# Performance work log

Measured on AMD Instinct MI355X. Metric: run time of the kernel, lower is better.

Reference implementation:

```python
import jax, jax.numpy as jnp
import numpy as np

N = 50000      # nodes
E = 800000     # edges (before self-loops)
F_IN = 128     # input node features
H = 4          # attention heads
C = 32         # hidden channels per head (concat width = H*C = 128)
CLS = 40       # num classes (layer 4, concat=False -> mean over heads)
NEG_SLOPE = 0.2


def setup_inputs() -> dict:
    key = jax.random.key(0)
    ks = jax.random.split(key, 16)
    w = lambda k, shape: (jax.random.normal(k, shape, jnp.float32) * 0.1)
    return {
        "x": jax.random.normal(ks[0], (N, F_IN), jnp.float32),
        "edge_index": jax.random.randint(ks[1], (2, E), 0, N),
        "W1": w(ks[2], (F_IN, H * C)), "att_src1": w(ks[3], (H, C)), "att_dst1": w(ks[4], (H, C)), "b1": jnp.zeros((H * C,), jnp.float32),
        "W2": w(ks[5], (H * C, H * C)), "att_src2": w(ks[6], (H, C)), "att_dst2": w(ks[7], (H, C)), "b2": jnp.zeros((H * C,), jnp.float32),
        "W3": w(ks[8], (H * C, H * C)), "att_src3": w(ks[9], (H, C)), "att_dst3": w(ks[10], (H, C)), "b3": jnp.zeros((H * C,), jnp.float32),
        "W4": w(ks[11], (H * C, H * CLS)), "att_src4": w(ks[12], (H, CLS)), "att_dst4": w(ks[13], (H, CLS)), "b4": jnp.zeros((CLS,), jnp.float32),
    }


def _gat(x, W, a_src, a_dst, b, src, dst, n, heads, ch, concat):
    # Linear transform, per-head view: [n, heads, ch]
    h = (x @ W).reshape(n, heads, ch)
    # per-node scalar attention terms [n, heads]
    es = (h * a_src).sum(-1)
    ed = (h * a_dst).sum(-1)
    # edge logits: alpha_j (source) + alpha_i (target), leaky relu (PyG GATConv)
    e = jax.nn.leaky_relu(es[src] + ed[dst], NEG_SLOPE)  # [Etot, heads]
    # segment softmax over incoming edges of each dst node (self-loops guarantee >=1 edge)
    m = jax.ops.segment_max(e, dst, num_segments=n)
    ealpha = jnp.exp(e - m[dst])
    denom = jax.ops.segment_sum(ealpha, dst, num_segments=n)
    alpha = ealpha / denom[dst]
    # weighted message aggregation (scatter-add)
    out = jax.ops.segment_sum(h[src] * alpha[:, :, None], dst, num_segments=n)
    out = out.reshape(n, heads * ch) if concat else out.mean(axis=1)
    return out + b


def reference(x, edge_index, W1, att_src1, att_dst1, b1, W2, att_src2, att_dst2, b2,
              W3, att_src3, att_dst3, b3, W4, att_src4, att_dst4, b4):
    n = x.shape[0]
    loop = jnp.arange(n)
    src = jnp.concatenate([edge_index[0], loop])  # add self-loops (PyG default)
    dst = jnp.concatenate([edge_index[1], loop])
    # dropout layers are identity in eval mode (training=False)
    h = _gat(x, W1, att_src1, att_dst1, b1, src, dst, n, H, C, True)
    h = jax.nn.relu(h)
    h = _gat(h, W2, att_src2, att_dst2, b2, src, dst, n, H, C, True)
    h = jax.nn.relu(h)
    h = _gat(h, W3, att_src3, att_dst3, b3, src, dst, n, H, C, True)
    h = jax.nn.relu(h)
    h = _gat(h, W4, att_src4, att_dst4, b4, src, dst, n, H, CLS, False)
    return h
```

## Files before the change

kernel.cpp:

```cpp
#include <hip/hip_runtime.h>
#include <math.h>

#define NN 50000
#define EE 800000
#define ET (EE + NN)
#define NCHK ((NN + 255) / 256)
#define NEG 0.2f

__device__ __forceinline__ float lrelu(float x) { return x > 0.f ? x : NEG * x; }

typedef __bf16 bf16x8 __attribute__((ext_vector_type(8)));
typedef float f32x4 __attribute__((ext_vector_type(4)));


__global__ __launch_bounds__(256) void k_init_cnt(int* cnt) {
    int i = blockIdx.x * 256 + threadIdx.x;
    if (i < NN) cnt[i] = 1;
}

__global__ __launch_bounds__(256) void k_hist(const int* __restrict__ eidx, int* __restrict__ cnt) {
    int i = blockIdx.x * 256 + threadIdx.x;
    if (i < EE) atomicAdd(&cnt[eidx[EE + i]], 1);
}

__global__ __launch_bounds__(256) void k_csum(const int* __restrict__ cnt, int* __restrict__ csums) {
    __shared__ int sh[256];
    int t = threadIdx.x, i = blockIdx.x * 256 + t;
    sh[t] = (i < NN) ? cnt[i] : 0;
    __syncthreads();
    for (int off = 128; off > 0; off >>= 1) {
        if (t < off) sh[t] += sh[t + off];
        __syncthreads();
    }
    if (t == 0) csums[blockIdx.x] = sh[0];
}

__global__ __launch_bounds__(256) void k_cscan(int* __restrict__ csums, int* __restrict__ rowptr) {
    __shared__ int sh[256];
    int t = threadIdx.x;
    sh[t] = (t < NCHK) ? csums[t] : 0;
    __syncthreads();
    for (int off = 1; off < 256; off <<= 1) {
        int x = (t >= off) ? sh[t - off] : 0;
        __syncthreads();
        sh[t] += x;
        __syncthreads();
    }
    int ex = (t == 0) ? 0 : sh[t - 1];
    if (t < NCHK) csums[t] = ex;
    if (t == 0) rowptr[NN] = ET;
}

__global__ __launch_bounds__(256) void k_chscan(const int* __restrict__ cnt, const int* __restrict__ csums,
                                                int* __restrict__ rowptr, int* __restrict__ cursor) {
    __shared__ int sh[256];
    int t = threadIdx.x, b = blockIdx.x, i = b * 256 + t;
    int v = (i < NN) ? cnt[i] : 0;
    sh[t] = v;
    __syncthreads();
    for (int off = 1; off < 256; off <<= 1) {
        int x = (t >= off) ? sh[t - off] : 0;
        __syncthreads();
        sh[t] += x;
        __syncthreads();
    }
    int ex = (t == 0 ? 0 : sh[t - 1]) + csums[b];
    if (i < NN) { rowptr[i] = ex; cursor[i] = ex; }
}

__global__ __launch_bounds__(256) void k_scatter(const int* __restrict__ eidx,
                                                 int* __restrict__ cursor, int* __restrict__ ssrc) {
    int i = blockIdx.x * 256 + threadIdx.x;
    if (i >= ET) return;
    int s, d;
    if (i < EE) { s = eidx[i]; d = eidx[EE + i]; } else { s = d = i - EE; }
    int pos = atomicAdd(&cursor[d], 1);
    ssrc[pos] = s;
}


template <int NOUT>
__global__ __launch_bounds__(256) void k_gemm_mfma(const float* __restrict__ X,
                                                   const float* __restrict__ Wm,
                                                   float* __restrict__ Y) {
    constexpr int NT = NOUT / 16;
    __shared__ __bf16 WH[4][NOUT][8];
    __shared__ __bf16 WL[4][NOUT][8];
    int tid = threadIdx.x;
    int w = tid >> 6, l = tid & 63;
    int rb = blockIdx.x * 64;
    int arow = rb + w * 16 + (l & 15);
    int rclamp = arow < NN ? arow : NN - 1;
    int kg = l >> 4;
    f32x4 acc[NT];
    #pragma unroll
    for (int t = 0; t < NT; ++t) acc[t] = (f32x4){0.f, 0.f, 0.f, 0.f};

    for (int kc = 0; kc < 128; kc += 32) {
        for (int idx = tid; idx < 32 * NOUT; idx += 256) {
            int kk = idx / NOUT;
            int c  = idx - kk * NOUT;
            float v = Wm[(size_t)(kc + kk) * NOUT + c];
            __bf16 hi = (__bf16)v;
            __bf16 lo = (__bf16)(v - (float)hi);
            WH[kk >> 3][c][kk & 7] = hi;
            WL[kk >> 3][c][kk & 7] = lo;
        }
        __syncthreads();

        float4 aA = *reinterpret_cast<const float4*>(&X[(size_t)rclamp * 128 + kc + kg * 8]);
        float4 aB = *reinterpret_cast<const float4*>(&X[(size_t)rclamp * 128 + kc + kg * 8 + 4]);
        float av[8] = {aA.x, aA.y, aA.z, aA.w, aB.x, aB.y, aB.z, aB.w};
        bf16x8 ahi, alo;
        #pragma unroll
        for (int j = 0; j < 8; ++j) {
            __bf16 h = (__bf16)av[j];
            ahi[j] = h;
            alo[j] = (__bf16)(av[j] - (float)h);
        }

        #pragma unroll
        for (int t = 0; t < NT; ++t) {
            bf16x8 bhi = *reinterpret_cast<const bf16x8*>(&WH[kg][t * 16 + (l & 15)][0]);
            bf16x8 blo = *reinterpret_cast<const bf16x8*>(&WL[kg][t * 16 + (l & 15)][0]);
            acc[t] = __builtin_amdgcn_mfma_f32_16x16x32_bf16(ahi, bhi, acc[t], 0, 0, 0);
            acc[t] = __builtin_amdgcn_mfma_f32_16x16x32_bf16(alo, bhi, acc[t], 0, 0, 0);
            acc[t] = __builtin_amdgcn_mfma_f32_16x16x32_bf16(ahi, blo, acc[t], 0, 0, 0);
        }
        __syncthreads();
    }

    #pragma unroll
    for (int t = 0; t < NT; ++t) {
        int cc = t * 16 + (l & 15);
        #pragma unroll
        for (int i = 0; i < 4; ++i) {
            int rr = rb + w * 16 + (l >> 4) * 4 + i;
            if (rr < NN) Y[(size_t)rr * NOUT + cc] = acc[t][i];
        }
    }
}


template <int CH>
__global__ __launch_bounds__(256) void k_attn_scal(const float* __restrict__ Hf,
                                                   const float* __restrict__ asrc,
                                                   const float* __restrict__ adst,
                                                   float* __restrict__ es, float* __restrict__ ed) {
    int i = blockIdx.x * 256 + threadIdx.x;
    if (i >= NN * 4) return;
    int h = i & 3, n = i >> 2;
    const float4* row = reinterpret_cast<const float4*>(Hf + (size_t)n * (4 * CH) + h * CH);
    const float4* As  = reinterpret_cast<const float4*>(asrc + h * CH);
    const float4* Ad  = reinterpret_cast<const float4*>(adst + h * CH);
    float s = 0.f, d = 0.f;
    #pragma unroll
    for (int c = 0; c < CH / 4; ++c) {
        float4 v = row[c], a = As[c], b = Ad[c];
        s += v.x * a.x + v.y * a.y + v.z * a.z + v.w * a.w;
        d += v.x * b.x + v.y * b.y + v.z * b.z + v.w * b.w;
    }
    es[i] = s;
    ed[i] = d;
}


__global__ __launch_bounds__(256) void k_agg128(const float* __restrict__ Hf,
                                                const float* __restrict__ es, const float* __restrict__ ed,
                                                const int* __restrict__ rowptr, const int* __restrict__ ssrc,
                                                const float* __restrict__ bias, float* __restrict__ Yout) {
    int wid = (blockIdx.x * 256 + threadIdx.x) >> 6;
    int lane = threadIdx.x & 63;
    if (wid >= NN) return;
    int n = wid;
    int beg = rowptr[n], end = rowptr[n + 1];
    int h1 = lane & 3;
    int eoff = lane >> 2;
    float edv = ed[n * 4 + h1];

    float m = -1e30f, dsum = 0.f;
    for (int idx = beg + eoff; idx < end; idx += 16) {
        int s = ssrc[idx];
        float e = lrelu(es[s * 4 + h1] + edv);
        float M = fmaxf(m, e);
        dsum = dsum * __expf(m - M) + __expf(e - M);
        m = M;
    }
    #pragma unroll
    for (int off = 4; off < 64; off <<= 1) {
        float om = __shfl_xor(m, off);
        float od = __shfl_xor(dsum, off);
        float M = fmaxf(m, om);
        dsum = dsum * __expf(m - M) + od * __expf(om - M);
        m = M;
    }
    float invd = 1.f / dsum;

    int q = lane & 7;
    int eg8 = lane >> 3;
    f32x4 acc4[4];
    #pragma unroll
    for (int i = 0; i < 4; ++i) acc4[i] = (f32x4){0.f, 0.f, 0.f, 0.f};

    int nch = (end - beg + 15) >> 4;
    int base = beg;
    for (int ch = 0; ch < nch; ++ch, base += 16) {
        int myIdx = base + eoff;
        int s = ssrc[myIdx < end ? myIdx : end - 1];
        float e = lrelu(es[s * 4 + h1] + edv);
        float alpha = (myIdx < end) ? __expf(e - m) * invd : 0.f;
        #pragma unroll
        for (int hb = 0; hb < 2; ++hb) {
            int e16 = hb * 8 + eg8;
            int se = __shfl(s, e16 * 4);
            const float* rowp = Hf + (size_t)se * 128 + q * 4;
            #pragma unroll
            for (int i = 0; i < 4; ++i) {
                float p = __shfl(alpha, e16 * 4 + i);
                float4 v = *reinterpret_cast<const float4*>(rowp + i * 32);
                acc4[i].x += p * v.x;
                acc4[i].y += p * v.y;
                acc4[i].z += p * v.z;
                acc4[i].w += p * v.w;
            }
        }
    }

    #pragma unroll
    for (int off = 8; off < 64; off <<= 1) {
        #pragma unroll
        for (int i = 0; i < 4; ++i) {
            acc4[i].x += __shfl_xor(acc4[i].x, off);
            acc4[i].y += __shfl_xor(acc4[i].y, off);
            acc4[i].z += __shfl_xor(acc4[i].z, off);
            acc4[i].w += __shfl_xor(acc4[i].w, off);
        }
    }
    if (lane < 8) {
        #pragma unroll
        for (int i = 0; i < 4; ++i) {
            int c0 = 32 * i + 4 * lane;
            float4 bv = *reinterpret_cast<const float4*>(&bias[c0]);
            float4 o;
            o.x = fmaxf(acc4[i].x + bv.x, 0.f);
            o.y = fmaxf(acc4[i].y + bv.y, 0.f);
            o.z = fmaxf(acc4[i].z + bv.z, 0.f);
            o.w = fmaxf(acc4[i].w + bv.w, 0.f);
            *reinterpret_cast<float4*>(&Yout[(size_t)n * 128 + c0]) = o;
        }
    }
}


__global__ __launch_bounds__(256) void k_agg160_mean(const float* __restrict__ Hf,
                                                     const float* __restrict__ es, const float* __restrict__ ed,
                                                     const int* __restrict__ rowptr, const int* __restrict__ ssrc,
                                                     const float* __restrict__ b4, float* __restrict__ out) {
    __shared__ float buf[4][160];
    int wid = (blockIdx.x * 256 + threadIdx.x) >> 6;
    int lane = threadIdx.x & 63;
    int w = threadIdx.x >> 6;
    if (wid >= NN) return;
    int n = wid;
    int beg = rowptr[n], end = rowptr[n + 1];
    int h1 = lane & 3;
    int eoff = lane >> 2;
    float edv = ed[n * 4 + h1];

    float m = -1e30f, dsum = 0.f;
    for (int idx = beg + eoff; idx < end; idx += 16) {
        int s = ssrc[idx];
        float e = lrelu(es[s * 4 + h1] + edv);
        float M = fmaxf(m, e);
        dsum = dsum * __expf(m - M) + __expf(e - M);
        m = M;
    }
    #pragma unroll
    for (int off = 4; off < 64; off <<= 1) {
        float om = __shfl_xor(m, off);
        float od = __shfl_xor(dsum, off);
        float M = fmaxf(m, om);
        dsum = dsum * __expf(m - M) + od * __expf(om - M);
        m = M;
    }
    float invd = 1.f / dsum;

    int q = lane & 7;
    int eg8 = lane >> 3;
    int hh[5];
    #pragma unroll
    for (int i = 0; i < 5; ++i) hh[i] = (i * 8 + q) / 10;
    f32x4 acc4[5];
    #pragma unroll
    for (int i = 0; i < 5; ++i) acc4[i] = (f32x4){0.f, 0.f, 0.f, 0.f};

    int nch = (end - beg + 15) >> 4;
    int base = beg;
    for (int ch = 0; ch < nch; ++ch, base += 16) {
        int myIdx = base + eoff;
        int s = ssrc[myIdx < end ? myIdx : end - 1];
        float e = lrelu(es[s * 4 + h1] + edv);
        float alpha = (myIdx < end) ? __expf(e - m) * invd : 0.f;
        #pragma unroll
        for (int hb = 0; hb < 2; ++hb) {
            int e16 = hb * 8 + eg8;
            int se = __shfl(s, e16 * 4);
            const float* rowp = Hf + (size_t)se * 160 + q * 4;
            #pragma unroll
            for (int i = 0; i < 5; ++i) {
                float p = __shfl(alpha, e16 * 4 + hh[i]);
                float4 v = *reinterpret_cast<const float4*>(rowp + i * 32);
                acc4[i].x += p * v.x;
                acc4[i].y += p * v.y;
                acc4[i].z += p * v.z;
                acc4[i].w += p * v.w;
            }
        }
    }

    #pragma unroll
    for (int off = 8; off < 64; off <<= 1) {
        #pragma unroll
        for (int i = 0; i < 5; ++i) {
            acc4[i].x += __shfl_xor(acc4[i].x, off);
            acc4[i].y += __shfl_xor(acc4[i].y, off);
            acc4[i].z += __shfl_xor(acc4[i].z, off);
            acc4[i].w += __shfl_xor(acc4[i].w, off);
        }
    }
    if (lane < 8) {
        #pragma unroll
        for (int i = 0; i < 5; ++i)
            *reinterpret_cast<float4*>(&buf[w][32 * i + 4 * lane]) = (float4){acc4[i].x, acc4[i].y, acc4[i].z, acc4[i].w};
    }
    __builtin_amdgcn_wave_barrier();
    if (lane < 40) {
        float v = 0.25f * (buf[w][lane] + buf[w][lane + 40] + buf[w][lane + 80] + buf[w][lane + 120]) + b4[lane];
        out[(size_t)n * 40 + lane] = v;
    }
}


extern "C" void kernel_launch(void* const* d_in, const int* in_sizes, int n_in,
                              void* d_out, int out_size, void* d_ws, size_t ws_size,
                              hipStream_t stream) {
    const float* x    = (const float*)d_in[0];
    const int*   eidx = (const int*)d_in[1];
    const float* W[4]    = {(const float*)d_in[2], (const float*)d_in[6], (const float*)d_in[10], (const float*)d_in[14]};
    const float* asrc[4] = {(const float*)d_in[3], (const float*)d_in[7], (const float*)d_in[11], (const float*)d_in[15]};
    const float* adst[4] = {(const float*)d_in[4], (const float*)d_in[8], (const float*)d_in[12], (const float*)d_in[16]};
    const float* bias[4] = {(const float*)d_in[5], (const float*)d_in[9], (const float*)d_in[13], (const float*)d_in[17]};
    float* out = (float*)d_out;

    float* hA = (float*)d_ws;
    float* hB = hA + (size_t)NN * 160;
    float* es = hB + (size_t)NN * 160;
    float* ed = es + (size_t)NN * 4;
    int* rowptr = (int*)(ed + (size_t)NN * 4);
    int* cnt    = rowptr + (NN + 1);
    int* cursor = cnt + NN;
    int* ssrc   = cursor + NN;
    int* csums  = ssrc + ET;

    k_init_cnt<<<(NN + 255) / 256, 256, 0, stream>>>(cnt);
    k_hist<<<(EE + 255) / 256, 256, 0, stream>>>(eidx, cnt);
    k_csum<<<NCHK, 256, 0, stream>>>(cnt, csums);
    k_cscan<<<1, 256, 0, stream>>>(csums, rowptr);
    k_chscan<<<NCHK, 256, 0, stream>>>(cnt, csums, rowptr, cursor);
    k_scatter<<<(ET + 255) / 256, 256, 0, stream>>>(eidx, cursor, ssrc);

    int gemmBlocks = (NN + 63) / 64;
    int aggBlocks = (NN * 64 + 255) / 256;

    k_gemm_mfma<128><<<gemmBlocks, 256, 0, stream>>>(x, W[0], hA);
    k_attn_scal<32><<<(NN * 4 + 255) / 256, 256, 0, stream>>>(hA, asrc[0], adst[0], es, ed);
    k_agg128<<<aggBlocks, 256, 0, stream>>>(hA, es, ed, rowptr, ssrc, bias[0], hB);

    k_gemm_mfma<128><<<gemmBlocks, 256, 0, stream>>>(hB, W[1], hA);
    k_attn_scal<32><<<(NN * 4 + 255) / 256, 256, 0, stream>>>(hA, asrc[1], adst[1], es, ed);
    k_agg128<<<aggBlocks, 256, 0, stream>>>(hA, es, ed, rowptr, ssrc, bias[1], hB);

    k_gemm_mfma<128><<<gemmBlocks, 256, 0, stream>>>(hB, W[2], hA);
    k_attn_scal<32><<<(NN * 4 + 255) / 256, 256, 0, stream>>>(hA, asrc[2], adst[2], es, ed);
    k_agg128<<<aggBlocks, 256, 0, stream>>>(hA, es, ed, rowptr, ssrc, bias[2], hB);

    k_gemm_mfma<160><<<gemmBlocks, 256, 0, stream>>>(hB, W[3], hA);
    k_attn_scal<40><<<(NN * 4 + 255) / 256, 256, 0, stream>>>(hA, asrc[3], adst[3], es, ed);
    k_agg160_mean<<<aggBlocks, 256, 0, stream>>>(hA, es, ed, rowptr, ssrc, bias[3], out);
}
```

Measured before the change: 510.1 us.

## Pre-split weights to bf16 hi/lo once and fuse attention scalars into GEMM epilogue

Weights are now split into bf16 hi/lo pairs by a small separate kernel per layer, so the GEMM blocks read them directly from global memory instead of each block reconverting them into shared memory behind barriers. For the first three layers the per-node attention dot products are computed in the GEMM epilogue using cross-lane shuffle reductions, which removes the separate attn_scal pass and its re-read of the features. The count initialisation kernel is replaced by a memset, with the self-loop +1 folded into the scan kernels. In exchange, B-operand loads now go through global memory and cache instead of LDS, and the shuffle reduction adds register pressure.

New measurement: 500.9 us. Within noise of the previous version (-1.8%).

```diff
diff --git a/kernel.cpp b/kernel.cpp
--- a/kernel.cpp
+++ b/kernel.cpp
@@ -13,11 +13,6 @@
 typedef float f32x4 __attribute__((ext_vector_type(4)));
 
 
-__global__ __launch_bounds__(256) void k_init_cnt(int* cnt) {
-    int i = blockIdx.x * 256 + threadIdx.x;
-    if (i < NN) cnt[i] = 1;
-}
-
 __global__ __launch_bounds__(256) void k_hist(const int* __restrict__ eidx, int* __restrict__ cnt) {
     int i = blockIdx.x * 256 + threadIdx.x;
     if (i < EE) atomicAdd(&cnt[eidx[EE + i]], 1);
@@ -26,7 +21,7 @@
 __global__ __launch_bounds__(256) void k_csum(const int* __restrict__ cnt, int* __restrict__ csums) {
     __shared__ int sh[256];
     int t = threadIdx.x, i = blockIdx.x * 256 + t;
-    sh[t] = (i < NN) ? cnt[i] : 0;
+    sh[t] = (i < NN) ? cnt[i] + 1 : 0;
     __syncthreads();
     for (int off = 128; off > 0; off >>= 1) {
         if (t < off) sh[t] += sh[t + off];
@@ -55,7 +50,7 @@
                                                 int* __restrict__ rowptr, int* __restrict__ cursor) {
     __shared__ int sh[256];
     int t = threadIdx.x, b = blockIdx.x, i = b * 256 + t;
-    int v = (i < NN) ? cnt[i] : 0;
+    int v = (i < NN) ? cnt[i] + 1 : 0;
     sh[t] = v;
     __syncthreads();
     for (int off = 1; off < 256; off <<= 1) {
@@ -80,36 +75,43 @@
 
 
 template <int NOUT>
-__global__ __launch_bounds__(256) void k_gemm_mfma(const float* __restrict__ X,
-                                                   const float* __restrict__ Wm,
-                                                   float* __restrict__ Y) {
+__global__ __launch_bounds__(256) void k_wsplit(const float* __restrict__ Wm,
+                                                __bf16* __restrict__ Whi, __bf16* __restrict__ Wlo) {
+    int i = blockIdx.x * 256 + threadIdx.x;
+    if (i >= 128 * NOUT) return;
+    int k = i / NOUT, c = i - k * NOUT;
+    float v = Wm[i];
+    __bf16 hi = (__bf16)v;
+    __bf16 lo = (__bf16)(v - (float)hi);
+    size_t off = ((size_t)(k >> 3) * NOUT + c) * 8 + (k & 7);
+    Whi[off] = hi;
+    Wlo[off] = lo;
+}
+
+
+template <int NOUT, bool FUSE>
+__global__ __launch_bounds__(256) void k_gemm2(const float* __restrict__ X,
+                                               const __bf16* __restrict__ Whi,
+                                               const __bf16* __restrict__ Wlo,
+                                               float* __restrict__ Y,
+                                               const float* __restrict__ asrc,
+                                               const float* __restrict__ adst,
+                                               float* __restrict__ es, float* __restrict__ ed) {
     constexpr int NT = NOUT / 16;
-    __shared__ __bf16 WH[4][NOUT][8];
-    __shared__ __bf16 WL[4][NOUT][8];
     int tid = threadIdx.x;
     int w = tid >> 6, l = tid & 63;
+    int col = l & 15, kg = l >> 4;
     int rb = blockIdx.x * 64;
-    int arow = rb + w * 16 + (l & 15);
+    int arow = rb + w * 16 + col;
     int rclamp = arow < NN ? arow : NN - 1;
-    int kg = l >> 4;
     f32x4 acc[NT];
     #pragma unroll
     for (int t = 0; t < NT; ++t) acc[t] = (f32x4){0.f, 0.f, 0.f, 0.f};
 
-    for (int kc = 0; kc < 128; kc += 32) {
-        for (int idx = tid; idx < 32 * NOUT; idx += 256) {
-            int kk = idx / NOUT;
-            int c  = idx - kk * NOUT;
-            float v = Wm[(size_t)(kc + kk) * NOUT + c];
-            __bf16 hi = (__bf16)v;
-            __bf16 lo = (__bf16)(v - (float)hi);
-            WH[kk >> 3][c][kk & 7] = hi;
-            WL[kk >> 3][c][kk & 7] = lo;
-        }
-        __syncthreads();
-
-        float4 aA = *reinterpret_cast<const float4*>(&X[(size_t)rclamp * 128 + kc + kg * 8]);
-        float4 aB = *reinterpret_cast<const float4*>(&X[(size_t)rclamp * 128 + kc + kg * 8 + 4]);
+    #pragma unroll
+    for (int c4 = 0; c4 < 4; ++c4) {
+        float4 aA = *reinterpret_cast<const float4*>(&X[(size_t)rclamp * 128 + c4 * 32 + kg * 8]);
+        float4 aB = *reinterpret_cast<const float4*>(&X[(size_t)rclamp * 128 + c4 * 32 + kg * 8 + 4]);
         float av[8] = {aA.x, aA.y, aA.z, aA.w, aB.x, aB.y, aB.z, aB.w};
         bf16x8 ahi, alo;
         #pragma unroll
@@ -118,25 +120,67 @@
             ahi[j] = h;
             alo[j] = (__bf16)(av[j] - (float)h);
         }
-
+        const __bf16* bh = Whi + ((size_t)(c4 * 4 + kg) * NOUT) * 8;
+        const __bf16* bl = Wlo + ((size_t)(c4 * 4 + kg) * NOUT) * 8;
         #pragma unroll
         for (int t = 0; t < NT; ++t) {
-            bf16x8 bhi = *reinterpret_cast<const bf16x8*>(&WH[kg][t * 16 + (l & 15)][0]);
-            bf16x8 blo = *reinterpret_cast<const bf16x8*>(&WL[kg][t * 16 + (l & 15)][0]);
+            bf16x8 bhi = *reinterpret_cast<const bf16x8*>(bh + (t * 16 + col) * 8);
+            bf16x8 blo = *reinterpret_cast<const bf16x8*>(bl + (t * 16 + col) * 8);
             acc[t] = __builtin_amdgcn_mfma_f32_16x16x32_bf16(ahi, bhi, acc[t], 0, 0, 0);
             acc[t] = __builtin_amdgcn_mfma_f32_16x16x32_bf16(alo, bhi, acc[t], 0, 0, 0);
             acc[t] = __builtin_amdgcn_mfma_f32_16x16x32_bf16(ahi, blo, acc[t], 0, 0, 0);
         }
-        __syncthreads();
     }
 
     #pragma unroll
     for (int t = 0; t < NT; ++t) {
-        int cc = t * 16 + (l & 15);
+        int cc = t * 16 + col;
         #pragma unroll
         for (int i = 0; i < 4; ++i) {
-            int rr = rb + w * 16 + (l >> 4) * 4 + i;
+            int rr = rb + w * 16 + kg * 4 + i;
             if (rr < NN) Y[(size_t)rr * NOUT + cc] = acc[t][i];
+        }
+    }
+
+    if constexpr (FUSE) {
+        float pes[4][4], ped[4][4];
+        #pragma unroll
+        for (int h = 0; h < 4; ++h)
+            #pragma unroll
+            for (int i = 0; i < 4; ++i) { pes[h][i] = 0.f; ped[h][i] = 0.f; }
+        #pragma unroll
+        for (int t = 0; t < 8; ++t) {
+            float as = asrc[t * 16 + col];
+            float ad = adst[t * 16 + col];
+            int h = t >> 1;
+            #pragma unroll
+            for (int i = 0; i < 4; ++i) {
+                pes[h][i] += acc[t][i] * as;
+                ped[h][i] += acc[t][i] * ad;
+            }
+        }
+        #pragma unroll
+        for (int off = 1; off < 16; off <<= 1) {
+            #pragma unroll
+            for (int h = 0; h < 4; ++h)
+                #pragma unroll
+                for (int i = 0; i < 4; ++i) {
+                    pes[h][i] += __shfl_xor(pes[h][i], off);
+                    ped[h][i] += __shfl_xor(ped[h][i], off);
+                }
+        }
+        if (col == 0) {
+            #pragma unroll
+            for (int i = 0; i < 4; ++i) {
+                int rr = rb + w * 16 + kg * 4 + i;
+                if (rr < NN) {
+                    #pragma unroll
+                    for (int h = 0; h < 4; ++h) {
+                        es[rr * 4 + h] = pes[h][i];
+                        ed[rr * 4 + h] = ped[h][i];
+                    }
+                }
+            }
         }
     }
 }
@@ -361,30 +405,42 @@
     int* cursor = cnt + NN;
     int* ssrc   = cursor + NN;
     int* csums  = ssrc + ET;
-
-    k_init_cnt<<<(NN + 255) / 256, 256, 0, stream>>>(cnt);
+    __bf16* wsp = (__bf16*)(csums + 256);
+    __bf16* Whi[4], *Wlo[4];
+    {
+        __bf16* p = wsp;
+        for (int i = 0; i < 4; ++i) {
+            int sz = 128 * (i == 3 ? 160 : 128);
+            Whi[i] = p; p += sz;
+            Wlo[i] = p; p += sz;
+        }
+    }
+
+    hipMemsetAsync(cnt, 0, NN * sizeof(int), stream);
     k_hist<<<(EE + 255) / 256, 256, 0, stream>>>(eidx, cnt);
     k_csum<<<NCHK, 256, 0, stream>>>(cnt, csums);
     k_cscan<<<1, 256, 0, stream>>>(csums, rowptr);
     k_chscan<<<NCHK, 256, 0, stream>>>(cnt, csums, rowptr, cursor);
     k_scatter<<<(ET + 255) / 256, 256, 0, stream>>>(eidx, cursor, ssrc);
 
+    k_wsplit<128><<<(128 * 128 + 255) / 256, 256, 0, stream>>>(W[0], Whi[0], Wlo[0]);
+    k_wsplit<128><<<(128 * 128 + 255) / 256, 256, 0, stream>>>(W[1], Whi[1], Wlo[1]);
+    k_wsplit<128><<<(128 * 128 + 255) / 256, 256, 0, stream>>>(W[2], Whi[2], Wlo[2]);
+    k_wsplit<160><<<(128 * 160 + 255) / 256, 256, 0, stream>>>(W[3], Whi[3], Wlo[3]);
+
     int gemmBlocks = (NN + 63) / 64;
     int aggBlocks = (NN * 64 + 255) / 256;
 
-    k_gemm_mfma<128><<<gemmBlocks, 256, 0, stream>>>(x, W[0], hA);
-    k_attn_scal<32><<<(NN * 4 + 255) / 256, 256, 0, stream>>>(hA, asrc[0], adst[0], es, ed);
+    k_gemm2<128, true><<<gemmBlocks, 256, 0, stream>>>(x, Whi[0], Wlo[0], hA, asrc[0], adst[0], es, ed);
     k_agg128<<<aggBlocks, 256, 0, stream>>>(hA, es, ed, rowptr, ssrc, bias[0], hB);
 
-    k_gemm_mfma<128><<<gemmBlocks, 256, 0, stream>>>(hB, W[1], hA);
-    k_attn_scal<32><<<(NN * 4 + 255) / 256, 256, 0, stream>>>(hA, asrc[1], adst[1], es, ed);
+    k_gemm2<128, true><<<gemmBlocks, 256, 0, stream>>>(hB, Whi[1], Wlo[1], hA, asrc[1], adst[1], es, ed);
     k_agg128<<<aggBlocks, 256, 0, stream>>>(hA, es, ed, rowptr, ssrc, bias[1], hB);
 
-    k_gemm_mfma<128><<<gemmBlocks, 256, 0, stream>>>(hB, W[2], hA);
-    k_attn_scal<32><<<(NN * 4 + 255) / 256, 256, 0, stream>>>(hA, asrc[2], adst[2], es, ed);
+    k_gemm2<128, true><<<gemmBlocks, 256, 0, stream>>>(hB, Whi[2], Wlo[2], hA, asrc[2], adst[2], es, ed);
     k_agg128<<<aggBlocks, 256, 0, stream>>>(hA, es, ed, rowptr, ssrc, bias[2], hB);
 
-    k_gemm_mfma<160><<<gemmBlocks, 256, 0, stream>>>(hB, W[3], hA);
+    k_gemm2<160, false><<<gemmBlocks, 256, 0, stream>>>(hB, Whi[3], Wlo[3], hA, nullptr, nullptr, nullptr, nullptr);
     k_attn_scal<40><<<(NN * 4 + 255) / 256, 256, 0, stream>>>(hA, asrc[3], adst[3], es, ed);
     k_agg160_mean<<<aggBlocks, 256, 0, stream>>>(hA, es, ed, rowptr, ssrc, bias[3], out);
 }
```
